# Optimization experiments

Measured on AMD Instinct MI355X. Metric: run time of the kernel, lower is better.

The kernel has to match this reference:

```python
import jax, jax.numpy as jnp
import numpy as np

L = 16          # num_sites
CHI_MAX = 64    # max bond dimension
VOCAB = 128000
TRUNC_EVERY = 10
DT = jnp.float32


def _mps_add(A, B):
    """Direct sum of two MPS (block-diagonal on bonds, boundaries concatenated)."""
    out = []
    for s in range(L):
        a, b = A[s], B[s]
        cla, d, cra = a.shape
        clb, _, crb = b.shape
        if s == 0:
            out.append(jnp.concatenate([a, b], axis=2))          # [1,d,cra+crb]
        elif s == L - 1:
            out.append(jnp.concatenate([a, b], axis=0))          # [cla+clb,d,1]
        else:
            t = jnp.zeros((cla + clb, d, cra + crb), a.dtype)
            t = t.at[:cla, :, :cra].set(a).at[cla:, :, cra:].set(b)
            out.append(t)
    return out


def _truncate(T, chi_max):
    """Left-to-right SVD sweep truncating every bond to <= chi_max."""
    T = list(T)
    for s in range(L - 1):
        cl, d, cr = T[s].shape
        U, S, Vh = jnp.linalg.svd(T[s].reshape(cl * d, cr), full_matrices=False)
        k = min(chi_max, int(S.shape[0]))
        T[s] = U[:, :k].reshape(cl, d, k)
        carry = S[:k, None] * Vh[:k]                              # [k, cr]
        T[s + 1] = jnp.einsum('kl,ldr->kdr', carry, T[s + 1])
    return T


def _forward(cores_hidden, cores_input, head_w, head_b, init_ctx, toks):
    # D=1 MPO core -> per-site 2x2 matrix acting on the physical index
    Wh = cores_hidden[:, 0, :, :, 0]   # [L,2,2]
    Wi = cores_input[:, 0, :, :, 0]    # [L,2,2]
    e0 = jnp.array([1.0, 0.0], DT).reshape(1, 2, 1)
    e1 = jnp.array([0.0, 1.0], DT).reshape(1, 2, 1)
    ctx = [init_ctx[s] for s in range(L)]
    for t, tok in enumerate(toks, start=1):
        bits = [(tok >> i) & 1 for i in range(L)]
        emb = [e1 if b else e0 for b in reversed(bits)]
        # h_{t+1} = W_hidden @ h_t  (+)  W_input @ embed(token)
        h = [jnp.einsum('ij,ljr->lir', Wh[s], ctx[s]) for s in range(L)]
        x = [jnp.einsum('ij,ljr->lir', Wi[s], emb[s]) for s in range(L)]
        ctx = _mps_add(h, x)
        if t % TRUNC_EVERY == 0 and ctx[0].shape[2] > CHI_MAX:
            ctx = _truncate(ctx, CHI_MAX)
    # predict(): mean of middle site over (left bond, phys) -> feature vector
    vec = ctx[L // 2].mean(axis=(0, 1))
    c = vec.shape[0]
    vec = jnp.pad(vec, (0, CHI_MAX - c)) if c < CHI_MAX else vec[:CHI_MAX]
    return head_w @ vec + head_b


def setup_inputs() -> dict:
    key = jax.random.key(0)
    k1, k2, k3, k4, k5, k6 = jax.random.split(key, 6)
    eye = jnp.eye(2, dtype=DT)
    cores_hidden = (0.02 * jax.random.normal(k1, (L, 1, 2, 2, 1), DT)).at[:, 0, :, :, 0].add(eye)
    cores_input = (0.02 * jax.random.normal(k2, (L, 1, 2, 2, 1), DT)).at[:, 0, :, :, 0].add(eye)
    head_w = jax.random.normal(k3, (VOCAB, CHI_MAX), DT) / jnp.sqrt(jnp.float32(CHI_MAX))
    head_b = 0.02 * jax.random.normal(k4, (VOCAB,), DT)
    init_ctx = jax.random.normal(k5, (L, 1, 2, 1), DT)
    token_ids = jax.random.randint(k6, (100,), 0, 65536, dtype=jnp.int32)
    return {"cores_hidden": cores_hidden, "cores_input": cores_input,
            "head_w": head_w, "head_b": head_b,
            "init_ctx": init_ctx, "token_ids": token_ids}


def reference(cores_hidden, cores_input, head_w, head_b, init_ctx, token_ids):
    toks = [int(t) for t in np.asarray(token_ids)]
    return _forward(cores_hidden, cores_input, head_w, head_b, init_ctx, toks)
```

## Files before the change

kernel.cpp:

```cpp
#include <hip/hip_runtime.h>

typedef double rl;
#define NT 256
#define NSV 71
#define LDA 128
#define LDV 72
#define SML 25
#define VOCAB 128000
#define LP 27
#define PB 129

#define EPS32 1.1920928955078125e-7
#define UNFL32 1.17549435e-38

#define O_CAR   0
#define O_COLS  4608
#define O_VEC   4800
#define O_MA    5120
#define O_MBLG  14208
#define O_MU    23552
#define O_MQ    32768
#define O_MVT   41984
#define O_SUB   47168
#define O_SVTB  52352
#define O_U2    57536
#define O_VT2   62720
#define O_QU    67904
#define O_QV    73088
#define O_TB    78272
#define O_D     83456
#define O_E     83528
#define O_TQ    83600
#define O_TP    83672

__device__ double g_ws[84000];

struct LeafCtx {
  rl LVT[26*LP], LU[26*LP];
  rl b1[26], b2[26], b3[26], b4[26];
  rl sc[6];
  int ia[26], ib[26], ic[26];
  int si[12];
};

struct Sh {
  rl d[72], e[72], tq[72], tp[72], rc[72], rs[72];
  rl dsig[72], zz[72], zh[72], sigm[72], vals[72];
  rl ta[72], tb[72];
  int srcU[72], srcVT[72], perm[72];
  int ia[72], ib[72], ic[72];
  int opk[12], opf[12], opa[12], opb[12], opq[12];
  rl sc[16];
  int si[24];
};

__device__ __forceinline__ void wsync(){
  asm volatile("s_waitcnt vmcnt(0) lgkmcnt(0)" ::: "memory");
}

__device__ __forceinline__ rl d_sign(rl a, rl b){ return (b >= 0.0) ? fabs(a) : -fabs(a); }
__device__ __forceinline__ rl dlapy2(rl x, rl y){
  rl ax=fabs(x), ay=fabs(y);
  rl w = ax>ay?ax:ay, z = ax>ay?ay:ax;
  if(z==0.0) return w;
  rl t = z/w; return w*sqrt(1.0+t*t);
}
__device__ void dlartg(rl f, rl g, rl* cs, rl* sn, rl* r){
  if(g==0.0){ *cs=1.0; *sn=0.0; *r=f; }
  else if(f==0.0){ *cs=0.0; *sn=d_sign(1.0,g); *r=fabs(g); }
  else{
    rl dd = sqrt(f*f+g*g);
    *cs = fabs(f)/dd;
    *r  = d_sign(dd, f);
    *sn = g/(*r);
  }
}

__device__ void dlas2(rl f, rl g, rl h, rl* ssmin, rl* ssmax){
  rl fa=fabs(f), ga=fabs(g), ha=fabs(h);
  rl fhmn=fmin(fa,ha), fhmx=fmax(fa,ha);
  if(fhmn==0.0){
    *ssmin=0.0;
    if(fhmx==0.0) *ssmax=ga;
    else { rl mx=fmax(fhmx,ga), mn=fmin(fhmx,ga); rl q=mn/mx; *ssmax=mx*sqrt(1.0+q*q); }
  } else {
    if(ga < fhmx){
      rl as=1.0+fhmn/fhmx, at=(fhmx-fhmn)/fhmx;
      rl au=(ga/fhmx); au=au*au;
      rl c=2.0/(sqrt(as*as+au)+sqrt(at*at+au));
      *ssmin=fhmn*c; *ssmax=fhmx/c;
    } else {
      rl au=fhmx/ga;
      if(au==0.0){ *ssmin=(fhmn*fhmx)/ga; *ssmax=ga; }
      else{
        rl as=1.0+fhmn/fhmx, at=(fhmx-fhmn)/fhmx;
        rl c=1.0/(sqrt(1.0+(as*au)*(as*au))+sqrt(1.0+(at*au)*(at*au)));
        *ssmin=(fhmn*c)*au; *ssmin=*ssmin+*ssmin;
        *ssmax=ga/(c+c);
      }
    }
  }
}

__device__ void dlasv2(rl f, rl g, rl h, rl* ssmin, rl* ssmax, rl* snr, rl* csr, rl* snl, rl* csl){
  rl ft=f, fa=fabs(f), ht=h, ha=fabs(h);
  int pmax=1;
  bool swp = (ha > fa);
  if(swp){ pmax=3; rl t=ft; ft=ht; ht=t; t=fa; fa=ha; ha=t; }
  rl gt=g, ga=fabs(g);
  rl clt=0, crt=0, slt=0, srt=0;
  if(ga==0.0){ *ssmin=ha; *ssmax=fa; clt=1.0; crt=1.0; slt=0.0; srt=0.0; }
  else{
    bool gasmal=true;
    if(ga > fa){
      pmax=2;
      if((fa/ga) < EPS32){
        gasmal=false;
        *ssmax=ga;
        if(ha>1.0) *ssmin=fa/(ga/ha); else *ssmin=(fa/ga)*ha;
        clt=1.0; slt=ht/gt; srt=1.0; crt=ft/gt;
      }
    }
    if(gasmal){
      rl dd=fa-ha;
      rl lv = (dd==fa) ? 1.0 : dd/fa;
      rl mq = gt/ft;
      rl tv = 2.0-lv;
      rl mm = mq*mq, tt = tv*tv;
      rl sv = sqrt(tt+mm);
      rl rv = (lv==0.0) ? fabs(mq) : sqrt(lv*lv+mm);
      rl a = 0.5*(sv+rv);
      *ssmin = ha/a; *ssmax = fa*a;
      rl t3;
      if(mm==0.0){
        if(lv==0.0) t3 = d_sign(2.0, ft)*d_sign(1.0, gt);
        else t3 = gt/d_sign(dd, ft) + mq/tv;
      } else {
        t3 = (mq/(sv+tv) + mq/(rv+lv))*(1.0+a);
      }
      rl l2 = sqrt(t3*t3+4.0);
      crt = 2.0/l2; srt = t3/l2;
      clt = (crt + srt*mq)/a;
      slt = (ht/ft)*srt/a;
    }
  }
  if(swp){ *csl=srt; *snl=crt; *csr=slt; *snr=clt; }
  else  { *csl=clt; *snl=slt; *csr=crt; *snr=srt; }
  rl tsign=1.0;
  if(pmax==1) tsign = d_sign(1.0,*csr)*d_sign(1.0,*csl)*d_sign(1.0,f);
  if(pmax==2) tsign = d_sign(1.0,*snr)*d_sign(1.0,*csl)*d_sign(1.0,g);
  if(pmax==3) tsign = d_sign(1.0,*snr)*d_sign(1.0,*snl)*d_sign(1.0,h);
  *ssmax = d_sign(*ssmax, tsign);
  *ssmin = d_sign(*ssmin, tsign*d_sign(1.0,f)*d_sign(1.0,h));
}

__device__ __forceinline__ void row_apply(rl* row, size_t ld, const rl* v, size_t vs, int len, rl tau){
  rl s = row[0];
  int i=0;
  for(; i+16<=len; i+=16){
    rl a[16], b[16];
    #pragma unroll
    for(int u=0;u<16;++u){ a[u]=row[ld*(size_t)(1+i+u)]; b[u]=v[vs*(size_t)(i+u)]; }
    #pragma unroll
    for(int u=0;u<16;++u) s += a[u]*b[u];
  }
  for(; i<len; ++i) s += row[ld*(size_t)(1+i)]*v[vs*(size_t)i];
  rl w = s*tau;
  row[0] -= w;
  i=0;
  for(; i+16<=len; i+=16){
    rl b[16];
    #pragma unroll
    for(int u=0;u<16;++u) b[u]=v[vs*(size_t)(i+u)];
    #pragma unroll
    for(int u=0;u<16;++u) row[ld*(size_t)(1+i+u)] -= w*b[u];
  }
  for(; i<len; ++i) row[ld*(size_t)(1+i)] -= w*v[vs*(size_t)i];
}

__device__ __forceinline__ void app_left_s(rl* A, int ld, int r0, int m, int c0, int n, const rl* vbase, rl scl, rl tau, int tid){
  const int len = m - r0 - 1;
  const rl* v = vbase + r0 + 1;
  int c = c0 + tid;
  if(c < n){
    rl* col = A + (size_t)ld*c + r0;
    rl s = col[0];
    int i=0;
    for(; i+16<=len; i+=16){
      rl a[16], b[16];
      #pragma unroll
      for(int u=0;u<16;++u){ a[u]=col[1+i+u]; b[u]=v[i+u]*scl; }
      #pragma unroll
      for(int u=0;u<16;++u) s += a[u]*b[u];
    }
    for(; i<len; ++i) s += col[1+i]*(v[i]*scl);
    rl w = s*tau;
    col[0] -= w;
    i=0;
    for(; i+16<=len; i+=16){
      rl b[16];
      #pragma unroll
      for(int u=0;u<16;++u) b[u]=v[i+u]*scl;
      #pragma unroll
      for(int u=0;u<16;++u) col[1+i+u] -= w*b[u];
    }
    for(; i<len; ++i) col[1+i] -= w*(v[i]*scl);
  }
}
__device__ __forceinline__ void app_right_s(rl* A, int ld, int r0, int m, int c0, int n, const rl* vbase, int vstride, rl scl, rl tau, int tid){
  const int len = n - c0 - 1;
  const rl* v = vbase + (size_t)vstride*(c0+1);
  int r = r0 + tid;
  if(r < m){
    rl* row = A + r + (size_t)ld*c0;
    rl s = row[0];
    int i=0;
    for(; i+16<=len; i+=16){
      rl a[16], b[16];
      #pragma unroll
      for(int u=0;u<16;++u){ a[u]=row[(size_t)ld*(size_t)(1+i+u)]; b[u]=v[(size_t)vstride*(size_t)(i+u)]*scl; }
      #pragma unroll
      for(int u=0;u<16;++u) s += a[u]*b[u];
    }
    for(; i<len; ++i) s += row[(size_t)ld*(1+i)]*(v[(size_t)vstride*i]*scl);
    rl w = s*tau;
    row[0] -= w;
    i=0;
    for(; i+16<=len; i+=16){
      rl b[16];
      #pragma unroll
      for(int u=0;u<16;++u) b[u]=v[(size_t)vstride*(size_t)(i+u)]*scl;
      #pragma unroll
      for(int u=0;u<16;++u) row[(size_t)ld*(size_t)(1+i+u)] -= w*b[u];
    }
    for(; i<len; ++i) row[(size_t)ld*(1+i)] -= w*(v[(size_t)vstride*i]*scl);
  }
}

__device__ void bdsqr_wave(int n, rl* d, rl* e, int ncvt, int nru, LeafCtx* lc, int lane){
  if(n>1){
    rl eps=EPS32, unfl=UNFL32;
    rl tolmul=fmax(10.0,fmin(100.0,pow(eps,-0.125)));
    rl tol=tolmul*eps;
    rl thresh=0.0;
    int mm=n-1, oldll=-2, oldm=-2, idir=0, iter=0, maxit=6*n*n;
    if(lane==0){
      rl sminoa=fabs(d[0]);
      if(sminoa!=0.0){
        rl mu=sminoa;
        for(int i=1;i<n;++i){ mu=fabs(d[i])*(mu/(mu+fabs(e[i-1]))); sminoa=fmin(sminoa,mu); if(sminoa==0.0)break; }
      }
      sminoa=sminoa/sqrt((rl)n);
      thresh=fmax(tol*sminoa,(rl)(6*n*n)*unfl);
    }
    while(true){
      if(lane==0){
        int act=0, p_lo=0, p_cnt=0, p_fwd=1, p_mm=0;
        while(mm>0){
          if(iter>maxit) break;
          rl smax=fabs(d[mm]), smin=smax;
          int ll=-1;
          for(int lll=mm-1;lll>=0;--lll){
            rl abss=fabs(d[lll]), abse=fabs(e[lll]);
            if(abse<=thresh){ ll=lll; break; }
            smin=fmin(smin,abss);
            smax=fmax(smax,fmax(abss,abse));
          }
          if(ll==mm-1){ e[ll]=0.0; mm=mm-1; continue; }
          if(ll>=0) e[ll]=0.0;
          int lo=ll+1;
          if(mm==lo+1){
            rl sigmn,sigmx,sinr,cosr,sinl,cosl;
            dlasv2(d[lo],e[lo],d[mm],&sigmn,&sigmx,&sinr,&cosr,&sinl,&cosl);
            d[lo]=sigmx; d[mm]=sigmn; e[lo]=0.0;
            lc->sc[0]=cosr; lc->sc[1]=sinr; lc->sc[2]=cosl; lc->sc[3]=sinl;
            act=2; p_lo=lo; p_mm=mm;
            mm-=2;
            break;
          }
          if(lo>oldm || mm<oldll) idir=(fabs(d[lo])>=fabs(d[mm]))?1:2;
          rl sminl=0.0; int conv=0;
          if(idir==1){
            if(fabs(e[mm-1])<=tol*fabs(d[mm])){ e[mm-1]=0.0; conv=1; }
            if(!conv){
              rl mu=fabs(d[lo]); sminl=mu;
              for(int lll=lo;lll<mm;++lll){
                if(fabs(e[lll])<=tol*mu){ e[lll]=0.0; conv=1; break; }
                mu=fabs(d[lll+1])*(mu/(mu+fabs(e[lll])));
                sminl=fmin(sminl,mu);
              }
            }
          } else {
            if(fabs(e[lo])<=tol*fabs(d[lo])){ e[lo]=0.0; conv=1; }
            if(!conv){
              rl mu=fabs(d[mm]); sminl=mu;
              for(int lll=mm-1;lll>=lo;--lll){
                if(fabs(e[lll])<=tol*mu){ e[lll]=0.0; conv=1; break; }
                mu=fabs(d[lll])*(mu/(mu+fabs(e[lll])));
                sminl=fmin(sminl,mu);
              }
            }
          }
          if(conv) continue;
          oldll=lo; oldm=mm;
          rl shift=0.0, rr_;
          if(!((rl)n*tol*(sminl/smax) <= fmax(eps, 0.01*tol))){
            rl sll;
            if(idir==1){ sll=fabs(d[lo]); dlas2(d[mm-1],e[mm-1],d[mm],&shift,&rr_); }
            else { sll=fabs(d[mm]); dlas2(d[lo],e[lo],d[lo+1],&shift,&rr_); }
            if(sll>0.0){ rl q=shift/sll; if(q*q<eps) shift=0.0; }
          }
          iter += mm-lo;
          int cnt=mm-lo;
          if(shift==0.0){
            if(idir==1){
              rl cs=1.0, oldcs=1.0, sn=0.0, oldsn=0.0, r;
              for(int i=lo;i<mm;++i){
                dlartg(d[i]*cs,e[i],&cs,&sn,&r);
                if(i>lo) e[i-1]=oldsn*r;
                dlartg(oldcs*r, d[i+1]*sn, &oldcs,&oldsn,&d[i]);
                lc->b1[i-lo]=cs; lc->b2[i-lo]=sn; lc->b3[i-lo]=oldcs; lc->b4[i-lo]=oldsn;
              }
              rl h=d[mm]*cs; d[mm]=h*oldcs; e[mm-1]=h*oldsn;
              p_fwd=1;
              if(fabs(e[mm-1])<=thresh) e[mm-1]=0.0;
            } else {
              rl cs=1.0, oldcs=1.0, sn=0.0, oldsn=0.0, r;
              for(int i=mm;i>lo;--i){
                dlartg(d[i]*cs,e[i-1],&cs,&sn,&r);
                if(i<mm) e[i]=oldsn*r;
                dlartg(oldcs*r,d[i-1]*sn,&oldcs,&oldsn,&d[i]);
                int j=i-lo-1;
                lc->b1[j]=oldcs; lc->b2[j]=-oldsn; lc->b3[j]=cs; lc->b4[j]=-sn;
              }
              rl h=d[lo]*cs; d[lo]=h*oldcs; e[lo]=h*oldsn;
              p_fwd=0;
              if(fabs(e[lo])<=thresh) e[lo]=0.0;
            }
          } else {
            if(idir==1){
              rl f2=(fabs(d[lo])-shift)*(d_sign(1.0,d[lo])+shift/d[lo]);
              rl g2=e[lo], r, cosr,sinr,cosl,sinl;
              for(int i=lo;i<mm;++i){
                dlartg(f2,g2,&cosr,&sinr,&r);
                if(i>lo) e[i-1]=r;
                f2=cosr*d[i]+sinr*e[i];
                e[i]=cosr*e[i]-sinr*d[i];
                g2=sinr*d[i+1];
                d[i+1]=cosr*d[i+1];
                dlartg(f2,g2,&cosl,&sinl,&r);
                d[i]=r;
                f2=cosl*e[i]+sinl*d[i+1];
                d[i+1]=cosl*d[i+1]-sinl*e[i];
                if(i<mm-1){ g2=sinl*e[i+1]; e[i+1]=cosl*e[i+1]; }
                lc->b1[i-lo]=cosr; lc->b2[i-lo]=sinr; lc->b3[i-lo]=cosl; lc->b4[i-lo]=sinl;
              }
              e[mm-1]=f2;
              p_fwd=1;
              if(fabs(e[mm-1])<=thresh) e[mm-1]=0.0;
            } else {
              rl f2=(fabs(d[mm])-shift)*(d_sign(1.0,d[mm])+shift/d[mm]);
              rl g2=e[mm-1], r, cosr,sinr,cosl,sinl;
              for(int i=mm;i>lo;--i){
                dlartg(f2,g2,&cosr,&sinr,&r);
                if(i<mm) e[i]=r;
                f2=cosr*d[i]+sinr*e[i-1];
                e[i-1]=cosr*e[i-1]-sinr*d[i];
                g2=sinr*d[i-1];
                d[i-1]=cosr*d[i-1];
                dlartg(f2,g2,&cosl,&sinl,&r);
                d[i]=r;
                f2=cosl*e[i-1]+sinl*d[i-1];
                d[i-1]=cosl*d[i-1]-sinl*e[i-1];
                if(i>lo+1){ g2=sinl*e[i-2]; e[i-2]=cosl*e[i-2]; }
                int j=i-lo-1;
                lc->b1[j]=cosl; lc->b2[j]=-sinl; lc->b3[j]=cosr; lc->b4[j]=-sinr;
              }
              e[lo]=f2;
              p_fwd=0;
              if(fabs(e[lo])<=thresh) e[lo]=0.0;
            }
          }
          act=1; p_lo=lo; p_cnt=cnt;
          break;
        }
        lc->si[7]=act; lc->si[8]=p_lo; lc->si[9]=p_cnt; lc->si[10]=p_fwd; lc->si[11]=p_mm;
      }
      wsync();
      int act=lc->si[7];
      if(act==0) break;
      if(act==1){
        int lo=lc->si[8], cnt=lc->si[9], fwd=lc->si[10];
        if(lane<ncvt){
          int k=lane;
          if(fwd){
            rl cur = lc->LVT[lo*LP+k];
            for(int j=0;j<cnt;++j){
              rl c=lc->b1[j], s=lc->b2[j];
              rl t = lc->LVT[(lo+j+1)*LP+k];
              lc->LVT[(lo+j)*LP+k] = s*t + c*cur;
              cur = c*t - s*cur;
            }
            lc->LVT[(lo+cnt)*LP+k] = cur;
          } else {
            rl tcar = lc->LVT[(lo+cnt)*LP+k];
            for(int j=cnt-1;j>=0;--j){
              rl c=lc->b1[j], s=lc->b2[j];
              rl low = lc->LVT[(lo+j)*LP+k];
              lc->LVT[(lo+j+1)*LP+k] = c*tcar - s*low;
              tcar = s*tcar + c*low;
            }
            lc->LVT[lo*LP+k] = tcar;
          }
        } else if(lane<ncvt+nru){
          int r2=lane-ncvt;
          if(fwd){
            rl cur = lc->LU[r2*LP+lo];
            for(int j=0;j<cnt;++j){
              rl c=lc->b3[j], s=lc->b4[j];
              rl t = lc->LU[r2*LP+(lo+j+1)];
              lc->LU[r2*LP+(lo+j)] = s*t + c*cur;
              cur = c*t - s*cur;
            }
            lc->LU[r2*LP+(lo+cnt)] = cur;
          } else {
            rl tcar = lc->LU[r2*LP+(lo+cnt)];
            for(int j=cnt-1;j>=0;--j){
              rl c=lc->b3[j], s=lc->b4[j];
              rl low = lc->LU[r2*LP+(lo+j)];
              lc->LU[r2*LP+(lo+j+1)] = c*tcar - s*low;
              tcar = s*tcar + c*low;
            }
            lc->LU[r2*LP+lo] = tcar;
          }
        }
      } else {
        int lo=lc->si[8], m2=lc->si[11];
        rl cosr=lc->sc[0], sinr=lc->sc[1], cosl=lc->sc[2], sinl=lc->sc[3];
        if(lane<ncvt){
          rl x=lc->LVT[lo*LP+lane], y=lc->LVT[m2*LP+lane];
          lc->LVT[lo*LP+lane]=cosr*x+sinr*y; lc->LVT[m2*LP+lane]=cosr*y-sinr*x;
        } else if(lane<ncvt+nru){
          int r2=lane-ncvt;
          rl x=lc->LU[r2*LP+lo], y=lc->LU[r2*LP+m2];
          lc->LU[r2*LP+lo]=cosl*x+sinl*y; lc->LU[r2*LP+m2]=cosl*y-sinl*x;
        }
      }
      wsync();
    }
  }
  if(lane==0){
    for(int i=0;i<n;++i){ lc->ic[i]=(d[i]<0.0)?1:0; if(d[i]<0.0) d[i]=-d[i]; }
    int nsw=0;
    for(int i=0;i<n-1;++i){
      int isub=0; rl smin=d[0];
      for(int j=1;j<n-i;++j){ if(d[j]<=smin){ isub=j; smin=d[j]; } }
      int tgt=n-1-i;
      if(isub!=tgt){
        d[isub]=d[tgt]; d[tgt]=smin;
        lc->ia[nsw]=isub; lc->ib[nsw]=tgt; ++nsw;
      }
    }
    lc->si[7]=nsw;
  }
  wsync();
  int nsw=lc->si[7];
  if(lane<ncvt){
    for(int i=0;i<n;++i) if(lc->ic[i]) lc->LVT[i*LP+lane]=-lc->LVT[i*LP+lane];
    for(int w2=0;w2<nsw;++w2){
      int a=lc->ia[w2], b=lc->ib[w2];
      rl t=lc->LVT[a*LP+lane]; lc->LVT[a*LP+lane]=lc->LVT[b*LP+lane]; lc->LVT[b*LP+lane]=t;
    }
  } else if(lane<ncvt+nru){
    int r2=lane-ncvt;
    for(int w2=0;w2<nsw;++w2){
      int a=lc->ia[w2], b=lc->ib[w2];
      rl t=lc->LU[r2*LP+a]; lc->LU[r2*LP+a]=lc->LU[r2*LP+b]; lc->LU[r2*LP+b]=t;
    }
  }
  wsync();
}

__device__ void leaf_exec(int f, int n, int sqre, int wantU, LeafCtx* lc, Sh* sh, int lane){
  rl* SVTB = g_ws + O_SVTB; rl* SUB = g_ws + O_SUB;
  int np = n + sqre;
  for(int w=lane; w<np*np; w+=64){ int r2=w/np, c=w-r2*np; lc->LVT[r2*LP+c]=SVTB[(f+r2)+(size_t)LDV*(f+c)]; }
  if(wantU) for(int w=lane; w<n*n; w+=64){ int r2=w/n, c=w-r2*n; lc->LU[r2*LP+c]=SUB[(f+r2)+(size_t)LDV*(f+c)]; }
  wsync();
  if(sqre==1){
    if(lane==0){
      rl cs,snv,rv; rl* dd=sh->d+f; rl* ee=sh->e+f;
      for(int i=0;i<n;++i){
        dlartg(dd[i],ee[i],&cs,&snv,&rv);
        dd[i]=rv;
        if(i<n-1){ ee[i]=snv*dd[i+1]; dd[i+1]=cs*dd[i+1]; }
        else ee[i]=0.0;
        lc->b1[i]=cs; lc->b2[i]=snv;
      }
    }
    wsync();
    if(lane<np){
      rl cur = lc->LVT[0*LP+lane];
      for(int j=0;j<n;++j){
        rl cj=lc->b1[j], sj=lc->b2[j];
        rl t=lc->LVT[(j+1)*LP+lane];
        lc->LVT[j*LP+lane] = sj*t + cj*cur;
        cur = cj*t - sj*cur;
      }
      lc->LVT[n*LP+lane] = cur;
    }
    wsync();
    if(lane==0){
      rl cs,snv,rv; rl* dd=sh->d+f; rl* ee=sh->e+f;
      for(int i=0;i<n-1;++i){
        dlartg(dd[i],ee[i],&cs,&snv,&rv);
        dd[i]=rv; ee[i]=snv*dd[i+1]; dd[i+1]=cs*dd[i+1];
        lc->b1[i]=cs; lc->b2[i]=snv;
      }
    }
    wsync();
    if(wantU && lane<n){
      rl cur = lc->LU[lane*LP+0];
      for(int j=0;j<n-1;++j){
        rl cj=lc->b1[j], sj=lc->b2[j];
        rl t=lc->LU[lane*LP+(j+1)];
        lc->LU[lane*LP+j] = sj*t + cj*cur;
        cur = cj*t - sj*cur;
      }
      lc->LU[lane*LP+(n-1)] = cur;
    }
    wsync();
  }
  bdsqr_wave(n, sh->d+f, sh->e+f, np, wantU? n:0, lc, lane);
  for(int w=lane; w<np*np; w+=64){ int r2=w/np, c=w-r2*np; SVTB[(f+r2)+(size_t)LDV*(f+c)]=lc->LVT[r2*LP+c]; }
  if(wantU) for(int w=lane; w<n*n; w+=64){ int r2=w/n, c=w-r2*n; SUB[(f+r2)+(size_t)LDV*(f+c)]=lc->LU[r2*LP+c]; }
}

__device__ void build_ops(int n, Sh* sh, int tid){
  if(tid==0){
    int sf[12], sn2[12], sq[12], sv[12]; int sp=0, no=0;
    sf[0]=0; sn2[0]=n; sq[0]=0; sv[0]=0; sp=1;
    while(sp>0){
      --sp;
      int f=sf[sp], nn=sn2[sp], q=sq[sp], v=sv[sp];
      if(nn<=SML){ sh->opk[no]=0; sh->opf[no]=f; sh->opa[no]=nn; sh->opb[no]=0; sh->opq[no]=q; ++no; }
      else if(v==0){
        int nl=nn/2, nr=nn-nl-1;
        sf[sp]=f; sn2[sp]=nn; sq[sp]=q; sv[sp]=1; ++sp;
        sf[sp]=f+nl+1; sn2[sp]=nr; sq[sp]=q; sv[sp]=0; ++sp;
        sf[sp]=f; sn2[sp]=nl; sq[sp]=1; sv[sp]=0; ++sp;
      } else {
        int nl=nn/2, nr=nn-nl-1;
        sh->opk[no]=1; sh->opf[no]=f; sh->opa[no]=nl; sh->opb[no]=nr; sh->opq[no]=q; ++no;
      }
    }
    int tk[12], tf2[12], ta2[12], tb3[12], tq3[12]; int c=0;
    for(int i=0;i<no;++i) if(sh->opk[i]==0){ tk[c]=0; tf2[c]=sh->opf[i]; ta2[c]=sh->opa[i]; tb3[c]=sh->opb[i]; tq3[c]=sh->opq[i]; ++c; }
    for(int i=0;i<no;++i) if(sh->opk[i]==1){ tk[c]=1; tf2[c]=sh->opf[i]; ta2[c]=sh->opa[i]; tb3[c]=sh->opb[i]; tq3[c]=sh->opq[i]; ++c; }
    for(int i=0;i<no;++i){ sh->opk[i]=tk[i]; sh->opf[i]=tf2[i]; sh->opa[i]=ta2[i]; sh->opb[i]=tb3[i]; sh->opq[i]=tq3[i]; }
    sh->si[6]=no;
  }
  __syncthreads();
}

__device__ void lasd1_merge2(int f, int nl, int nr, int sqre, int wantU,
                             rl* QVL, int qofs, int base, Sh* sh, int ltid, int lnt){
  rl* SUB = g_ws + O_SUB; rl* SVTB = g_ws + O_SVTB;
  rl* U2 = g_ws + O_U2; rl* VT2 = g_ws + O_VT2; rl* QU = g_ws + O_QU;
  rl* sc = sh->sc + (base?8:0);
  int* si = sh->si + (base?16:0);
  int n = nl+nr+1, m = n+sqre;
  {
    rl alpha = sh->d[f+nl], beta = sh->e[f+nl];
    if(ltid==0){
      sc[0]=alpha; sc[1]=beta;
      sh->vals[base]=0.0;
      sh->zz[base] = alpha*SVTB[(f+nl)+(size_t)LDV*(f+nl)];
      sh->srcU[base]=-1; sh->srcVT[base]=f+nl;
    } else if(ltid<n){
      int i=ltid;
      if(i<=nl){
        sh->vals[base+i]=sh->d[f+i-1];
        sh->zz[base+i]=alpha*SVTB[(f+i-1)+(size_t)LDV*(f+nl)];
        sh->srcU[base+i]=f+i-1; sh->srcVT[base+i]=f+i-1;
      } else {
        int j=i-1-nl;
        sh->vals[base+i]=sh->d[f+nl+1+j];
        sh->zz[base+i]=beta*SVTB[(f+nl+1+j)+(size_t)LDV*(f+nl+1)];
        sh->srcU[base+i]=f+nl+1+j; sh->srcVT[base+i]=f+nl+1+j;
      }
    }
  }
  __syncthreads();
  if(ltid==0 && sqre==1){
    rl zM = sc[1]*SVTB[(f+n)+(size_t)LDV*(f+nl+1)];
    rl c,s2,r2;
    dlartg(sh->zz[base], zM, &c, &s2, &r2);
    sh->zz[base]=r2; sc[2]=c; sc[3]=s2;
  }
  __syncthreads();
  if(sqre==1){
    rl c=sc[2], s=sc[3];
    int ra=f+nl, rb=f+n;
    for(int k=ltid;k<m;k+=lnt){
      size_t ci=(size_t)LDV*(f+k);
      rl a=SVTB[ra+ci], b=SVTB[rb+ci];
      SVTB[ra+ci]=c*a+s*b; SVTB[rb+ci]=-s*a+c*b;
    }
  }
  __syncthreads();
  if(ltid==0){
    rl maxd=0.0; for(int i=0;i<n;++i) maxd=fmax(maxd,fabs(sh->vals[base+i]));
    rl tol = 8.0*EPS32*fmax(maxd, fmax(fabs(sc[0]), fabs(sc[1])));
    sc[5]=tol;
    int Kc=0;
    for(int j=1;j<n;++j) if(fabs(sh->zz[base+j]) > tol) ++Kc;
    sh->ic[base]=0;
    si[0]=1+Kc; si[1]=n; si[2]=m; si[3]=f; si[4]=nl;
  }
  __syncthreads();
  {
    rl tol=sc[5];
    if(ltid>=1 && ltid<n){
      bool ndt = fabs(sh->zz[base+ltid])>tol;
      rl vt = sh->vals[base+ltid];
      int rank=0, Kc=0;
      for(int j=1;j<n;++j){
        bool ndj = fabs(sh->zz[base+j])>tol;
        if(ndj) ++Kc;
        if(ndj==ndt){
          rl vj=sh->vals[base+j];
          if(vj<vt || (vj==vt && j<ltid)) ++rank;
        }
      }
      int pos = ndt ? (1+rank) : (1+Kc+rank);
      sh->ic[base+pos]=ltid;
    }
  }
  __syncthreads();
  int K=si[0], n_=si[1], m_=si[2], f_=si[3], nl_=si[4];
  if(ltid<n_){ sh->ta[base+ltid]=sh->vals[base+ltid]; sh->tb[base+ltid]=sh->zz[base+ltid]; sh->ia[base+ltid]=sh->srcU[base+ltid]; sh->ib[base+ltid]=sh->srcVT[base+ltid]; }
  __syncthreads();
  if(ltid<n_){
    int p=sh->ic[base+ltid];
    sh->dsig[base+ltid]=sh->ta[base+p]; sh->zz[base+ltid]=sh->tb[base+p]; sh->srcU[base+ltid]=sh->ia[base+p]; sh->srcVT[base+ltid]=sh->ib[base+p];
  }
  __syncthreads();
  if(ltid==0){
    rl rho=0.0; for(int t=0;t<K;++t){ rl zv=sh->zz[base+t]; rho += zv*zv; }
    sc[4]=rho;
  }
  if(wantU){
    for(int w=ltid; w<n_*n_; w+=lnt){
      int col=w/n_, row=w-col*n_;
      int su=sh->srcU[base+col];
      rl v;
      if(su<0) v = (row==nl_) ? 1.0 : 0.0;
      else v = SUB[(f_+row)+(size_t)LDV*su];
      U2[(base+row)+(size_t)LDV*(base+col)]=v;
    }
  }
  for(int w=ltid; w<n_*m_; w+=lnt){
    int row=w/m_, col=w-row*m_;
    VT2[(base+row)+(size_t)LDV*(base+col)] = SVTB[sh->srcVT[base+row]+(size_t)LDV*(f_+col)];
  }
  __syncthreads();
  {
    rl rho=sc[4];
    if(ltid<K){
      int j=ltid;
      rl lo=sh->dsig[base+j];
      rl hi=(j<K-1)? sh->dsig[base+j+1] : sqrt(sh->dsig[base+K-1]*sh->dsig[base+K-1]+rho);
      for(int it=0; it<130; ++it){
        rl mid=0.5*(lo+hi);
        if(mid<=lo || mid>=hi) break;
        rl g=1.0;
        for(int i2=0;i2<K;++i2){
          rl zi=sh->zz[base+i2];
          g += zi*zi/((sh->dsig[base+i2]-mid)*(sh->dsig[base+i2]+mid));
        }
        if(g<0.0) lo=mid; else hi=mid;
      }
      sh->sigm[base+j]=0.5*(lo+hi);
    }
  }
  __syncthreads();
  if(ltid<K){
    int i2=ltid;
    rl di=sh->dsig[base+i2];
    rl p=(di - sh->sigm[base+K-1])*(di + sh->sigm[base+K-1]);
    for(int j=0;j<i2;++j)
      p *= (di - sh->sigm[base+j])*(di + sh->sigm[base+j])/((di - sh->dsig[base+j])*(di + sh->dsig[base+j]));
    for(int j=i2;j<K-1;++j)
      p *= (di - sh->sigm[base+j])*(di + sh->sigm[base+j])/((di - sh->dsig[base+j+1])*(di + sh->dsig[base+j+1]));
    sh->zh[base+i2] = d_sign(sqrt(fabs(p)), sh->zz[base+i2]);
  }
  __syncthreads();
  if(ltid<K){
    int j=ltid;
    rl sj=sh->sigm[base+j];
    rl nu=0.0, nv=0.0;
    for(int i2=0;i2<K;++i2){
      rl di=sh->dsig[base+i2];
      rl vv=sh->zh[base+i2]/((di-sj)*(di+sj));
      QVL[i2+(size_t)LDV*(j+qofs)]=vv; nv+=vv*vv;
      if(wantU){
        rl uu=(i2==0)? -1.0 : di*vv;
        QU[i2+(size_t)LDV*(j+qofs)]=uu; nu+=uu*uu;
      }
    }
    nv=1.0/sqrt(nv);
    for(int i2=0;i2<K;++i2) QVL[i2+(size_t)LDV*(j+qofs)]*=nv;
    if(wantU){
      nu=1.0/sqrt(nu);
      for(int i2=0;i2<K;++i2) QU[i2+(size_t)LDV*(j+qofs)]*=nu;
    }
  }
  __syncthreads();
  if(ltid==0){
    int nd2=n_-K;
    for(int t=0;t<nd2;++t) sh->ia[base+t]=K+t;
    int ps=K-1, pd=nd2-1;
    int t=0;
    while(t<n_){
      rl vs = (ps>=0)? sh->sigm[base+ps] : -1.0;
      rl vd = (pd>=0)? sh->dsig[base+sh->ia[base+pd]] : -1.0;
      if(vs >= vd){ sh->perm[base+t]=ps; sh->vals[base+t]=vs; --ps; }
      else { sh->perm[base+t]=1000+sh->ia[base+pd]; sh->vals[base+t]=vd; --pd; }
      ++t;
    }
  }
  __syncthreads();
  if(ltid<n_) sh->d[f_+ltid]=sh->vals[base+ltid];
  if(wantU){
    for(int w=ltid; w<n_*n_; w+=lnt){
      int t=w/n_, row=w-t*n_;
      int src=sh->perm[base+t];
      rl acc;
      if(src>=1000) acc = U2[(base+row)+(size_t)LDV*(base+(src-1000))];
      else{
        const rl* urow = U2 + (base+row) + (size_t)LDV*base;
        const rl* qcol = QU + (size_t)LDV*(src+qofs);
        rl s=0.0; int i=0;
        for(; i+16<=K; i+=16){
          rl a[16], b[16];
          #pragma unroll
          for(int u=0;u<16;++u){ a[u]=urow[(size_t)LDV*(size_t)(i+u)]; b[u]=qcol[i+u]; }
          #pragma unroll
          for(int u=0;u<16;++u) s += a[u]*b[u];
        }
        for(; i<K; ++i) s += urow[(size_t)LDV*i]*qcol[i];
        acc=s;
      }
      SUB[(f_+row)+(size_t)LDV*(f_+t)] = acc;
    }
  }
  for(int w=ltid; w<n_*m_; w+=lnt){
    int t=w/m_, col=w-t*m_;
    int src=sh->perm[base+t];
    rl acc;
    if(src>=1000) acc = VT2[(base+(src-1000))+(size_t)LDV*(base+col)];
    else{
      const rl* qcol = QVL + (size_t)LDV*(src+qofs);
      const rl* vcol = VT2 + base + (size_t)LDV*(base+col);
      rl s=0.0; int i=0;
      for(; i+16<=K; i+=16){
        rl a[16], b[16];
        #pragma unroll
        for(int u=0;u<16;++u){ a[u]=qcol[i+u]; b[u]=vcol[i+u]; }
        #pragma unroll
        for(int u=0;u<16;++u) s += a[u]*b[u];
      }
      for(; i<K; ++i) s += qcol[i]*vcol[i];
      acc=s;
    }
    SVTB[(f_+t)+(size_t)LDV*(f_+col)] = acc;
  }
  __syncthreads();
}

__device__ __forceinline__ void gebd2_upper(rl* A, int ld, int m, int n, Sh* sh, int tid){
  const int lane = tid & 63;
  rl pend_scl = 0.0; int pend_ds = 0;
  for(int i=0;i<n;++i){
    rl ps=0.0;
    for(int r=i+1+lane;r<m;r+=64){ rl vv=A[r+(size_t)ld*i]; ps+=vv*vv; }
    for(int off=32;off>0;off>>=1) ps += __shfl_xor(ps,off,64);
    rl alpha=A[i+(size_t)ld*i];
    rl xn=sqrt(ps);
    rl beta,tau,scl; int ds;
    if(xn==0.0){ tau=0.0; beta=alpha; scl=0.0; ds=0; }
    else{ beta=-d_sign(dlapy2(alpha,xn),alpha); tau=(beta-alpha)/beta; scl=1.0/(alpha-beta); ds=1; }
    if(tid==0){ sh->d[i]=beta; sh->tq[i]=tau; }
    if(tau!=0.0)
      app_left_s(A, ld, i, m, i+1, n, A+(size_t)ld*i, scl, tau, tid);
    if(pend_ds && tid>=128){
      int c = i+1 + (tid-128);
      if(c < n) A[(i-1)+(size_t)ld*c] *= pend_scl;
    }
    __syncthreads();
    if(i<n-1){
      rl ps2=0.0;
      for(int c=i+2+lane;c<n;c+=64){ rl vv=A[i+(size_t)ld*c]; ps2+=vv*vv; }
      for(int off=32;off>0;off>>=1) ps2 += __shfl_xor(ps2,off,64);
      rl alpha2=A[i+(size_t)ld*(i+1)];
      rl xn2=sqrt(ps2);
      rl beta2,tau2,scl2; int ds2;
      if(xn2==0.0){ tau2=0.0; beta2=alpha2; scl2=0.0; ds2=0; }
      else{ beta2=-d_sign(dlapy2(alpha2,xn2),alpha2); tau2=(beta2-alpha2)/beta2; scl2=1.0/(alpha2-beta2); ds2=1; }
      if(tid==0){ sh->e[i]=beta2; sh->tp[i]=tau2; }
      if(tau2!=0.0)
        app_right_s(A, ld, i+1, m, i+1, n, A+i, ld, scl2, tau2, tid);
      if(ds && tid>=128){
        int r = i+1 + (tid-128);
        if(r < m) A[r+(size_t)ld*i] *= scl;
      }
      pend_ds = ds2; pend_scl = scl2;
      __syncthreads();
    } else {
      if(tid==0) sh->tp[i]=0.0;
      __syncthreads();
      if(ds) for(int r=i+1+tid; r<m; r+=NT) A[r+(size_t)ld*(n-1)] *= scl;
      __syncthreads();
    }
  }
}

__device__ __forceinline__ void gebd2_lower(rl* A, int ld, int m, int n, Sh* sh, int tid){
  const int lane = tid & 63;
  rl pend_scl = 0.0; int pend_ds = 0;
  int last_ds = 0; rl last_scl = 0.0;
  for(int i=0;i<m;++i){
    rl ps=0.0;
    for(int c=i+1+lane;c<n;c+=64){ rl vv=A[i+(size_t)ld*c]; ps+=vv*vv; }
    for(int off=32;off>0;off>>=1) ps += __shfl_xor(ps,off,64);
    rl alpha=A[i+(size_t)ld*i];
    rl xn=sqrt(ps);
    rl beta,tau,scl; int ds;
    if(xn==0.0){ tau=0.0; beta=alpha; scl=0.0; ds=0; }
    else{ beta=-d_sign(dlapy2(alpha,xn),alpha); tau=(beta-alpha)/beta; scl=1.0/(alpha-beta); ds=1; }
    if(tid==0){ sh->d[i]=beta; sh->tp[i]=tau; }
    if(tau!=0.0)
      app_right_s(A, ld, i+1, m, i, n, A+i, ld, scl, tau, tid);
    if(pend_ds && tid>=128){
      int r = i+1 + (tid-128);
      if(r < m) A[r+(size_t)ld*(i-1)] *= pend_scl;
    }
    __syncthreads();
    if(i<m-1){
      rl ps2=0.0;
      for(int r=i+2+lane;r<m;r+=64){ rl vv=A[r+(size_t)ld*i]; ps2+=vv*vv; }
      for(int off=32;off>0;off>>=1) ps2 += __shfl_xor(ps2,off,64);
      rl alpha2=A[(i+1)+(size_t)ld*i];
      rl xn2=sqrt(ps2);
      rl beta2,tau2,scl2; int ds2;
      if(xn2==0.0){ tau2=0.0; beta2=alpha2; scl2=0.0; ds2=0; }
      else{ beta2=-d_sign(dlapy2(alpha2,xn2),alpha2); tau2=(beta2-alpha2)/beta2; scl2=1.0/(alpha2-beta2); ds2=1; }
      if(tid==0){ sh->e[i]=beta2; sh->tq[i]=tau2; }
      if(tau2!=0.0)
        app_left_s(A, ld, i+1, m, i+1, n, A+(size_t)ld*i, scl2, tau2, tid);
      if(ds && tid>=128){
        int c = i+1 + (tid-128);
        if(c < n) A[i+(size_t)ld*c] *= scl;
      }
      pend_ds = ds2; pend_scl = scl2;
      __syncthreads();
    } else {
      last_ds = ds; last_scl = scl;
      __syncthreads();
      if(last_ds) for(int c=i+1+tid; c<n; c+=NT) A[(m-1)+(size_t)ld*c] *= last_scl;
      __syncthreads();
    }
  }
}

__device__ __forceinline__ void gelq2(rl* A, int ld, int m, int n, Sh* sh, int tid){
  const int lane = tid & 63;
  rl pend_scl=0.0, pend_beta=0.0; int pend_ds=0;
  for(int i=0;i<m;++i){
    rl ps=0.0;
    for(int c=i+1+lane;c<n;c+=64){ rl vv=A[i+(size_t)ld*c]; ps+=vv*vv; }
    for(int off=32;off>0;off>>=1) ps += __shfl_xor(ps,off,64);
    rl alpha=A[i+(size_t)ld*i];
    rl xn=sqrt(ps);
    rl beta,tau,scl; int ds;
    if(xn==0.0){ tau=0.0; beta=alpha; scl=0.0; ds=0; }
    else{ beta=-d_sign(dlapy2(alpha,xn),alpha); tau=(beta-alpha)/beta; scl=1.0/(alpha-beta); ds=1; }
    if(tid==0) sh->rs[i]=tau;
    if(i<m-1 && tau!=0.0)
      app_right_s(A, ld, i+1, m, i, n, A+i, ld, scl, tau, tid);
    if(i>0 && tid>=128){
      if(pend_ds){ int c = i + (tid-128); if(c<n) A[(i-1)+(size_t)ld*c] *= pend_scl; }
      if(tid==128) A[(i-1)+(size_t)ld*(i-1)] = pend_beta;
    }
    pend_ds=ds; pend_scl=scl; pend_beta=beta;
    __syncthreads();
  }
  if(tid>=128){
    if(pend_ds){ int c = m + (tid-128); if(c<n) A[(m-1)+(size_t)ld*c] *= pend_scl; }
    if(tid==128) A[(m-1)+(size_t)ld*(m-1)] = pend_beta;
  }
  __syncthreads();
}

__global__ __launch_bounds__(NT)
void k_front(const float* __restrict__ ch, const float* __restrict__ ci,
             const float* __restrict__ ictx, const int* __restrict__ tok,
             int s, int m)
{
  __shared__ Sh sh;
  __shared__ LeafCtx lct[4];
  extern __shared__ rl MBL[];
  int tid = threadIdx.x;
  rl* MA = g_ws + O_MA; rl* MQ = g_ws + O_MQ; rl* TB = g_ws + O_TB;
  if(tid==0){
    rl W00=ch[s*4+0], W01=ch[s*4+1], W10=ch[s*4+2], W11=ch[s*4+3];
    rl P00=1,P01=0,P10=0,P11=1;
    for(int mexp=0;mexp<=70;++mexp){
      int j=70-mexp;
      rl v0,v1;
      if(j==0){ v0=ictx[s*2+0]; v1=ictx[s*2+1]; }
      else{
        int b=(tok[j-1]>>(15-s))&1;
        v0=ci[s*4+b]; v1=ci[s*4+2+b];
      }
      g_ws[O_COLS + 0 + 2*j] = P00*v0+P01*v1;
      g_ws[O_COLS + 1 + 2*j] = P10*v0+P11*v1;
      rl n00=W00*P00+W01*P10, n01=W00*P01+W01*P11;
      rl n10=W10*P00+W11*P10, n11=W10*P01+W11*P11;
      P00=n00;P01=n01;P10=n10;P11=n11;
    }
  }
  __syncthreads();
  for(int w=tid; w<m*NSV; w+=NT){
    int j=w/m, r2=w-j*m;
    int l=r2>>1, dd2=r2&1;
    rl cv = g_ws[O_COLS + dd2 + 2*j];
    MA[r2+(size_t)LDA*j] = (s==0)? cv : g_ws[O_CAR + l + 64*j]*cv;
  }
  __syncthreads();
  if(m==128){
    for(int w=tid;w<128*NSV;w+=NT){ int c=w>>7, r2=w&127; MBL[r2+(size_t)PB*c]=MA[r2+(size_t)LDA*c]; }
    __syncthreads();
    gebd2_upper(MBL, PB, 128, NSV, &sh, tid);
    for(int w=tid;w<PB*NSV;w+=NT) g_ws[O_MBLG+w]=MBL[w];
  } else if(m==64){
    for(int w=tid;w<64*NSV;w+=NT){ int c=w>>6, r2=w&63; MBL[r2+(size_t)PB*c]=MA[r2+(size_t)LDA*c]; }
    __syncthreads();
    gebd2_lower(MBL, PB, 64, NSV, &sh, tid);
    for(int w=tid;w<PB*NSV;w+=NT) g_ws[O_MBLG+w]=MBL[w];
    __syncthreads();
    if(tid==0){
      for(int i=0;i<63;++i){
        rl cs,snv,rv;
        dlartg(sh.d[i], sh.e[i], &cs,&snv,&rv);
        sh.d[i]=rv; sh.e[i]=snv*sh.d[i+1]; sh.d[i+1]=cs*sh.d[i+1];
      }
    }
  } else {
    for(int w=tid;w<m*NSV;w+=NT){ int c=w/m, r2=w-c*m; MBL[r2+(size_t)PB*c]=MA[r2+(size_t)LDA*c]; }
    __syncthreads();
    gelq2(MBL, PB, m, NSV, &sh, tid);
    for(int w=tid;w<m*NSV;w+=NT){ int c=w/m, r2=w-c*m; MQ[r2+(size_t)LDA*c]=(r2==c)?1.0:0.0; }
    __syncthreads();
    if(tid<m){
      int r=tid;
      for(int j=m-1;j>=0;--j){
        rl tau=sh.rs[j];
        if(tau!=0.0) row_apply(MQ + r + (size_t)LDA*j, LDA, MBL + j + (size_t)PB*(j+1), PB, NSV-j-1, tau);
      }
    }
    __syncthreads();
    for(int w=tid;w<m*m;w+=NT){ int c=w/m, r2=w-c*m; TB[r2+(size_t)LDV*c]=(r2>=c)? MBL[r2+(size_t)PB*c]:0.0; }
    __syncthreads();
    gebd2_upper(TB, LDV, m, m, &sh, tid);
  }
  __syncthreads();
  int wantU = (s==8)?1:0;
  int n_eff = (m==128)? NSV : m;
  rl* SUB = g_ws + O_SUB; rl* SVTB = g_ws + O_SVTB;
  for(int w=tid; w<LDV*LDV; w+=NT){
    int c=w/LDV, r2=w-c*LDV; rl v=(r2==c)?1.0:0.0;
    SVTB[w]=v;
    if(wantU) SUB[w]=v;
  }
  __syncthreads();
  if(n_eff<=SML){
    if((tid>>6)==0) leaf_exec(0, n_eff, 0, wantU, &lct[0], &sh, tid&63);
    __syncthreads();
  } else {
    build_ops(n_eff, &sh, tid);
    int no=sh.si[6];
    int o=0;
    while(o<no && sh.opk[o]==0){
      int cnt=1;
      while(o+cnt<no && sh.opk[o+cnt]==0 && cnt<4) ++cnt;
      int wid = tid>>6;
      if(wid<cnt) leaf_exec(sh.opf[o+wid], sh.opa[o+wid], sh.opq[o+wid], wantU, &lct[wid], &sh, tid&63);
      __syncthreads();
      o += cnt;
    }
  }
  if(tid<72){
    g_ws[O_D+tid]=sh.d[tid]; g_ws[O_E+tid]=sh.e[tid];
    g_ws[O_TQ+tid]=sh.tq[tid]; g_ws[O_TP+tid]=sh.tp[tid];
  }
}

__global__ __launch_bounds__(NT)
void k_back(const float* __restrict__ ch, int s, int m)
{
  __shared__ Sh sh;
  __shared__ rl QV[(size_t)LDV*72];
  extern __shared__ rl MBL[];
  int tid = threadIdx.x;
  rl* MU=g_ws+O_MU; rl* MVT=g_ws+O_MVT; rl* MQ=g_ws+O_MQ;
  rl* SUB=g_ws+O_SUB; rl* SVTB=g_ws+O_SVTB; rl* TB=g_ws+O_TB; rl* VT2=g_ws+O_VT2;
  if(tid<72){
    sh.d[tid]=g_ws[O_D+tid]; sh.e[tid]=g_ws[O_E+tid];
    sh.tq[tid]=g_ws[O_TQ+tid]; sh.tp[tid]=g_ws[O_TP+tid];
  }
  __syncthreads();
  int wantU = (s==8)?1:0;
  int n_eff = (m==128)? NSV : m;
  if(n_eff > SML){
    build_ops(n_eff, &sh, tid);
    int no=sh.si[6];
    int mstart=0; while(mstart<no && sh.opk[mstart]==0) ++mstart;
    int nm = no - mstart;
    if(nm==3){
      int slot = tid>>7, ltid = tid&127;
      int o = mstart + slot;
      lasd1_merge2(sh.opf[o], sh.opa[o], sh.opb[o], sh.opq[o], wantU,
                   QV, 36*slot, 36*slot, &sh, ltid, 128);
      int r = mstart+2;
      lasd1_merge2(sh.opf[r], sh.opa[r], sh.opb[r], sh.opq[r], wantU,
                   QV, 0, 0, &sh, tid, NT);
    } else {
      for(int o=mstart;o<no;++o)
        lasd1_merge2(sh.opf[o], sh.opa[o], sh.opb[o], sh.opq[o], wantU,
                     QV, 0, 0, &sh, tid, NT);
    }
  }
  __syncthreads();
  int k = (m<64)? m : 64;
  if(m==128){
    if(s==8){
      for(int w=tid;w<128*NSV;w+=NT){ int c=w>>7, r2=w&127; MU[r2+(size_t)LDA*c]=(r2<NSV)? SUB[r2+(size_t)LDV*c]:0.0; }
      for(int w=tid;w<PB*NSV;w+=NT) MBL[w]=g_ws[O_MBLG+w];
      __syncthreads();
      if(tid<NSV){
        int c=tid;
        rl* colb = MU + (size_t)LDA*c;
        for(int i=NSV-1;i>=0;--i){
          rl tau=sh.tq[i];
          if(tau!=0.0) row_apply(colb+i, 1, MBL + (size_t)PB*i + i + 1, 1, 128-i-1, tau);
        }
      }
      __syncthreads();
      if(tid==0){
        rl W00=ch[8*4+0], W01=ch[8*4+1], W10=ch[8*4+2], W11=ch[8*4+3];
        rl P00=1,P01=0,P10=0,P11=1;
        for(int it=0;it<30;++it){
          rl n00=W00*P00+W01*P10, n01=W00*P01+W01*P11;
          rl n10=W10*P00+W11*P10, n11=W10*P01+W11*P11;
          P00=n00;P01=n01;P10=n10;P11=n11;
        }
        sh.sc[0]=P00+P10; sh.sc[1]=P01+P11;
      }
      __syncthreads();
      for(int r2=tid; r2<64; r2+=NT){
        rl acc=0.0;
        for(int l=0;l<64;++l)
          acc += sh.sc[0]*MU[(2*l)+(size_t)LDA*r2] + sh.sc[1]*MU[(2*l+1)+(size_t)LDA*r2];
        g_ws[O_VEC + r2] = acc/188.0;
      }
    } else {
      for(int w=tid;w<LDV*NSV;w+=NT) MVT[w]=SVTB[w];
      for(int w=tid;w<PB*NSV;w+=NT) MBL[w]=g_ws[O_MBLG+w];
      __syncthreads();
      if(tid<NSV){
        int r=tid;
        for(int i=NSV-2;i>=0;--i){
          rl tau=sh.tp[i];
          if(tau!=0.0) row_apply(MVT + r + (size_t)LDV*(i+1), LDV, MBL + i + (size_t)PB*(i+2), PB, NSV-i-2, tau);
        }
      }
      __syncthreads();
      for(int w=tid; w<k*NSV; w+=NT){
        int j=w/k, l=w-j*k;
        g_ws[O_CAR + l + 64*j] = sh.d[l]*MVT[l+(size_t)LDV*j];
      }
    }
  } else if(m==64){
    for(int w=tid;w<64*NSV;w+=NT){ int c=w>>6, r2=w&63; MVT[r2+(size_t)LDV*c]=(c<64)? SVTB[r2+(size_t)LDV*c]:0.0; }
    for(int w=tid;w<PB*NSV;w+=NT) MBL[w]=g_ws[O_MBLG+w];
    __syncthreads();
    if(tid<64){
      int r=tid;
      for(int i=63;i>=0;--i){
        rl tau=sh.tp[i];
        if(tau!=0.0) row_apply(MVT + r + (size_t)LDV*i, LDV, MBL + i + (size_t)PB*(i+1), PB, NSV-i-1, tau);
      }
    }
    __syncthreads();
    for(int w=tid; w<k*NSV; w+=NT){
      int j=w/k, l=w-j*k;
      g_ws[O_CAR + l + 64*j] = sh.d[l]*MVT[l+(size_t)LDV*j];
    }
  } else {
    for(int w=tid;w<m*m;w+=NT){ int c=w/m, r2=w-c*m; VT2[r2+(size_t)LDV*c]=SVTB[r2+(size_t)LDV*c]; }
    __syncthreads();
    if(tid<m){
      int r=tid;
      for(int i=m-2;i>=0;--i){
        rl tau=sh.tp[i];
        if(tau!=0.0) row_apply(VT2 + r + (size_t)LDV*(i+1), LDV, TB + i + (size_t)LDV*(i+2), LDV, m-i-2, tau);
      }
    }
    __syncthreads();
    for(int w=tid;w<m*NSV;w+=NT){
      int c=w/m, r2=w-c*m;
      const rl* vrow = VT2 + r2;
      const rl* qcol = MQ + (size_t)LDA*c;
      rl s2=0.0; int t=0;
      for(; t+16<=m; t+=16){
        rl a[16], b[16];
        #pragma unroll
        for(int u=0;u<16;++u){ a[u]=vrow[(size_t)LDV*(size_t)(t+u)]; b[u]=qcol[t+u]; }
        #pragma unroll
        for(int u=0;u<16;++u) s2 += a[u]*b[u];
      }
      for(; t+4<=m; t+=4){
        rl a0=vrow[(size_t)LDV*t], a1=vrow[(size_t)LDV*(t+1)], a2=vrow[(size_t)LDV*(t+2)], a3=vrow[(size_t)LDV*(t+3)];
        rl b0=qcol[t], b1=qcol[t+1], b2=qcol[t+2], b3=qcol[t+3];
        s2+=a0*b0; s2+=a1*b1; s2+=a2*b2; s2+=a3*b3;
      }
      for(; t<m; ++t) s2 += vrow[(size_t)LDV*t]*qcol[t];
      MVT[r2+(size_t)LDV*c]=s2;
    }
    __syncthreads();
    for(int w=tid; w<k*NSV; w+=NT){
      int j=w/k, l=w-j*k;
      g_ws[O_CAR + l + 64*j] = sh.d[l]*MVT[l+(size_t)LDV*j];
    }
  }
}

__global__ __launch_bounds__(NT)
void head_kernel(const float* __restrict__ hw, const float* __restrict__ hb,
                 float* __restrict__ out)
{
  __shared__ float v[64];
  int tid=threadIdx.x;
  if(tid<64) v[tid]=(float)g_ws[O_VEC + tid];
  __syncthreads();
  int i = blockIdx.x*NT + tid;
  if(i<VOCAB){
    const float4* row = (const float4*)(hw + (size_t)i*64);
    float acc=0.f;
    #pragma unroll
    for(int c4=0;c4<16;++c4){
      float4 r4=row[c4];
      acc += r4.x*v[4*c4] + r4.y*v[4*c4+1] + r4.z*v[4*c4+2] + r4.w*v[4*c4+3];
    }
    out[i]=acc+hb[i];
  }
}

extern "C" void kernel_launch(void* const* d_in, const int* in_sizes, int n_in,
                              void* d_out, int out_size, void* d_ws, size_t ws_size,
                              hipStream_t stream)
{
  const float* ch  = (const float*)d_in[0];
  const float* ci  = (const float*)d_in[1];
  const float* hw  = (const float*)d_in[2];
  const float* hb  = (const float*)d_in[3];
  const float* ict = (const float*)d_in[4];
  const int*   tk  = (const int*)d_in[5];
  (void)d_ws; (void)ws_size; (void)in_sizes; (void)n_in; (void)out_size;

  static const int ms[9] = {2,4,8,16,32,64,128,128,128};
  size_t dynls = (size_t)PB*NSV*sizeof(double);
  for(int s=0;s<9;++s){
    hipLaunchKernelGGL(k_front, dim3(1), dim3(NT), dynls, stream, ch, ci, ict, tk, s, ms[s]);
    hipLaunchKernelGGL(k_back,  dim3(1), dim3(NT), dynls, stream, ch, s, ms[s]);
  }
  hipLaunchKernelGGL(head_kernel, dim3((VOCAB+NT-1)/NT), dim3(NT), 0, stream,
                     hw, hb, (float*)d_out);
}
```

Before: 7.319 ms.

## Fuse front and back SVD stage kernels, keep bidiagonal in LDS

Merges k_front and k_back into a single k_stage kernel per site, so the Householder-reflector matrix MBL and the d/e/tau vectors stay in shared memory rather than being round-tripped through the global workspace. This removes nine kernel launches and the global spill and reload of the MBL block. The merge-stage scratch QV now aliases the leaf-context shared buffer, which lowers LDS use but depends on the leaf phase having finished. It also precomputes z_i^2 once for the bisection secular-equation loop.

```diff
diff --git a/kernel.cpp b/kernel.cpp
--- a/kernel.cpp
+++ b/kernel.cpp
@@ -17,7 +17,6 @@
 #define O_COLS  4608
 #define O_VEC   4800
 #define O_MA    5120
-#define O_MBLG  14208
 #define O_MU    23552
 #define O_MQ    32768
 #define O_MVT   41984
@@ -26,12 +25,7 @@
 #define O_U2    57536
 #define O_VT2   62720
 #define O_QU    67904
-#define O_QV    73088
 #define O_TB    78272
-#define O_D     83456
-#define O_E     83528
-#define O_TQ    83600
-#define O_TP    83672
 
 __device__ double g_ws[84000];
 
@@ -650,6 +644,7 @@
     rl rho=0.0; for(int t=0;t<K;++t){ rl zv=sh->zz[base+t]; rho += zv*zv; }
     sc[4]=rho;
   }
+  if(ltid<K){ rl zi=sh->zz[base+ltid]; sh->tb[base+ltid]=zi*zi; }
   if(wantU){
     for(int w=ltid; w<n_*n_; w+=lnt){
       int col=w/n_, row=w-col*n_;
@@ -676,8 +671,7 @@
         if(mid<=lo || mid>=hi) break;
         rl g=1.0;
         for(int i2=0;i2<K;++i2){
-          rl zi=sh->zz[base+i2];
-          g += zi*zi/((sh->dsig[base+i2]-mid)*(sh->dsig[base+i2]+mid));
+          g += sh->tb[base+i2]/((sh->dsig[base+i2]-mid)*(sh->dsig[base+i2]+mid));
         }
         if(g<0.0) lo=mid; else hi=mid;
       }
@@ -904,7 +898,7 @@
 }
 
 __global__ __launch_bounds__(NT)
-void k_front(const float* __restrict__ ch, const float* __restrict__ ci,
+void k_stage(const float* __restrict__ ch, const float* __restrict__ ci,
              const float* __restrict__ ictx, const int* __restrict__ tok,
              int s, int m)
 {
@@ -913,6 +907,8 @@
   extern __shared__ rl MBL[];
   int tid = threadIdx.x;
   rl* MA = g_ws + O_MA; rl* MQ = g_ws + O_MQ; rl* TB = g_ws + O_TB;
+  rl* MU=g_ws+O_MU; rl* MVT=g_ws+O_MVT;
+  rl* SUB=g_ws+O_SUB; rl* SVTB=g_ws+O_SVTB; rl* VT2=g_ws+O_VT2;
   if(tid==0){
     rl W00=ch[s*4+0], W01=ch[s*4+1], W10=ch[s*4+2], W11=ch[s*4+3];
     rl P00=1,P01=0,P10=0,P11=1;
@@ -943,12 +939,10 @@
     for(int w=tid;w<128*NSV;w+=NT){ int c=w>>7, r2=w&127; MBL[r2+(size_t)PB*c]=MA[r2+(size_t)LDA*c]; }
     __syncthreads();
     gebd2_upper(MBL, PB, 128, NSV, &sh, tid);
-    for(int w=tid;w<PB*NSV;w+=NT) g_ws[O_MBLG+w]=MBL[w];
   } else if(m==64){
     for(int w=tid;w<64*NSV;w+=NT){ int c=w>>6, r2=w&63; MBL[r2+(size_t)PB*c]=MA[r2+(size_t)LDA*c]; }
     __syncthreads();
     gebd2_lower(MBL, PB, 64, NSV, &sh, tid);
-    for(int w=tid;w<PB*NSV;w+=NT) g_ws[O_MBLG+w]=MBL[w];
     __syncthreads();
     if(tid==0){
       for(int i=0;i<63;++i){
@@ -978,7 +972,6 @@
   __syncthreads();
   int wantU = (s==8)?1:0;
   int n_eff = (m==128)? NSV : m;
-  rl* SUB = g_ws + O_SUB; rl* SVTB = g_ws + O_SVTB;
   for(int w=tid; w<LDV*LDV; w+=NT){
     int c=w/LDV, r2=w-c*LDV; rl v=(r2==c)?1.0:0.0;
     SVTB[w]=v;
@@ -1000,45 +993,20 @@
       __syncthreads();
       o += cnt;
     }
-  }
-  if(tid<72){
-    g_ws[O_D+tid]=sh.d[tid]; g_ws[O_E+tid]=sh.e[tid];
-    g_ws[O_TQ+tid]=sh.tq[tid]; g_ws[O_TP+tid]=sh.tp[tid];
-  }
-}
-
-__global__ __launch_bounds__(NT)
-void k_back(const float* __restrict__ ch, int s, int m)
-{
-  __shared__ Sh sh;
-  __shared__ rl QV[(size_t)LDV*72];
-  extern __shared__ rl MBL[];
-  int tid = threadIdx.x;
-  rl* MU=g_ws+O_MU; rl* MVT=g_ws+O_MVT; rl* MQ=g_ws+O_MQ;
-  rl* SUB=g_ws+O_SUB; rl* SVTB=g_ws+O_SVTB; rl* TB=g_ws+O_TB; rl* VT2=g_ws+O_VT2;
-  if(tid<72){
-    sh.d[tid]=g_ws[O_D+tid]; sh.e[tid]=g_ws[O_E+tid];
-    sh.tq[tid]=g_ws[O_TQ+tid]; sh.tp[tid]=g_ws[O_TP+tid];
-  }
-  __syncthreads();
-  int wantU = (s==8)?1:0;
-  int n_eff = (m==128)? NSV : m;
-  if(n_eff > SML){
-    build_ops(n_eff, &sh, tid);
-    int no=sh.si[6];
-    int mstart=0; while(mstart<no && sh.opk[mstart]==0) ++mstart;
+    rl* QV = (rl*)lct;
+    int mstart=o;
     int nm = no - mstart;
     if(nm==3){
       int slot = tid>>7, ltid = tid&127;
-      int o = mstart + slot;
-      lasd1_merge2(sh.opf[o], sh.opa[o], sh.opb[o], sh.opq[o], wantU,
+      int oo = mstart + slot;
+      lasd1_merge2(sh.opf[oo], sh.opa[oo], sh.opb[oo], sh.opq[oo], wantU,
                    QV, 36*slot, 36*slot, &sh, ltid, 128);
       int r = mstart+2;
       lasd1_merge2(sh.opf[r], sh.opa[r], sh.opb[r], sh.opq[r], wantU,
                    QV, 0, 0, &sh, tid, NT);
     } else {
-      for(int o=mstart;o<no;++o)
-        lasd1_merge2(sh.opf[o], sh.opa[o], sh.opb[o], sh.opq[o], wantU,
+      for(int oo=mstart;oo<no;++oo)
+        lasd1_merge2(sh.opf[oo], sh.opa[oo], sh.opb[oo], sh.opq[oo], wantU,
                      QV, 0, 0, &sh, tid, NT);
     }
   }
@@ -1047,7 +1015,6 @@
   if(m==128){
     if(s==8){
       for(int w=tid;w<128*NSV;w+=NT){ int c=w>>7, r2=w&127; MU[r2+(size_t)LDA*c]=(r2<NSV)? SUB[r2+(size_t)LDV*c]:0.0; }
-      for(int w=tid;w<PB*NSV;w+=NT) MBL[w]=g_ws[O_MBLG+w];
       __syncthreads();
       if(tid<NSV){
         int c=tid;
@@ -1077,7 +1044,6 @@
       }
     } else {
       for(int w=tid;w<LDV*NSV;w+=NT) MVT[w]=SVTB[w];
-      for(int w=tid;w<PB*NSV;w+=NT) MBL[w]=g_ws[O_MBLG+w];
       __syncthreads();
       if(tid<NSV){
         int r=tid;
@@ -1094,7 +1060,6 @@
     }
   } else if(m==64){
     for(int w=tid;w<64*NSV;w+=NT){ int c=w>>6, r2=w&63; MVT[r2+(size_t)LDV*c]=(c<64)? SVTB[r2+(size_t)LDV*c]:0.0; }
-    for(int w=tid;w<PB*NSV;w+=NT) MBL[w]=g_ws[O_MBLG+w];
     __syncthreads();
     if(tid<64){
       int r=tid;
@@ -1183,8 +1148,7 @@
   static const int ms[9] = {2,4,8,16,32,64,128,128,128};
   size_t dynls = (size_t)PB*NSV*sizeof(double);
   for(int s=0;s<9;++s){
-    hipLaunchKernelGGL(k_front, dim3(1), dim3(NT), dynls, stream, ch, ci, ict, tk, s, ms[s]);
-    hipLaunchKernelGGL(k_back,  dim3(1), dim3(NT), dynls, stream, ch, s, ms[s]);
+    hipLaunchKernelGGL(k_stage, dim3(1), dim3(NT), dynls, stream, ch, ci, ict, tk, s, ms[s]);
   }
   hipLaunchKernelGGL(head_kernel, dim3((VOCAB+NT-1)/NT), dim3(NT), 0, stream,
                      hw, hb, (float*)d_out);
```

Result: no change. 7.192 ms (-1.7%).
